# Kernel tuning notes

Hardware: AMD Instinct MI355X
Metric: run time of the kernel (lower is better)

Reference implementation:

```python
import jax, jax.numpy as jnp
import numpy as np

T_STEPS, BATCH, DX, DH = 128, 128, 1024, 1024
N_GATES = 5


def setup_inputs() -> dict:
    key = jax.random.key(0)
    ks = jax.random.split(key, 4)
    scale_x = 1.0 / np.sqrt(DX)
    scale_h = 1.0 / np.sqrt(DH)
    inputs = jax.random.normal(ks[0], (T_STEPS, BATCH, DX), dtype=jnp.float32)
    memories = jax.random.normal(ks[1], (T_STEPS, BATCH, DH), dtype=jnp.float32)
    h0 = jnp.zeros((BATCH, DH), dtype=jnp.float32)
    c0 = jnp.zeros((BATCH, DH), dtype=jnp.float32)
    Wx = jax.random.normal(ks[2], (N_GATES * DH, DX), dtype=jnp.float32) * scale_x
    bx = jnp.zeros((N_GATES * DH,), dtype=jnp.float32)
    Wh = jax.random.normal(ks[3], (N_GATES * DH, DH), dtype=jnp.float32) * scale_h
    # forget-gate bias (second chunk) initialized to 1, as in reset_parameters_
    bh = jnp.zeros((N_GATES * DH,), dtype=jnp.float32).at[DH:2 * DH].set(1.0)
    return {"inputs": inputs, "memories": memories, "h0": h0, "c0": c0,
            "Wx": Wx, "bx": bx, "Wh": Wh, "bh": bh}


def reference(inputs, memories, h0, c0, Wx, bx, Wh, bh):
    # EpLSTMCell.loop: time-major scan of the custom gated cell.
    # Gate order: I, F, G, O, R (tied forget gate: it = 1 - ft).
    def step(carry, inp):
        h, c = carry
        xt, mt = inp
        gx = jnp.dot(xt, Wx.T) + bx      # [B, 5*Dh]
        gh = jnp.dot(h, Wh.T) + bh       # [B, 5*Dh]
        Xi, Xf, Xg, Xo, Xr = jnp.split(gx, N_GATES, axis=-1)
        Hi, Hf, Hg, Ho, Hr = jnp.split(gh, N_GATES, axis=-1)
        ft = jax.nn.sigmoid(Xf + Hf)
        ot = jax.nn.sigmoid(Xo + Ho)
        it = 1.0 - ft                    # tied forget gate
        gt = jnp.tanh(Xg + Hg)
        rt = jax.nn.sigmoid(Xr + Hr)     # episodic memory gate
        ct = ft * c + it * gt + rt * jnp.tanh(mt)
        ht = ot * jnp.tanh(ct)
        return (ht, ct), ht

    (_, _), outs = jax.lax.scan(step, (h0, c0), (inputs, memories))
    return outs  # [T, B, Dh]
```

## Files before the change

kernel.cpp:

```cpp
#include <hip/hip_runtime.h>

#define T_STEPS 128
#define BATCH   128
#define DX      1024
#define DH      1024
#define BDH     (BATCH * DH)
#define BDX     (BATCH * DX)

typedef __attribute__((ext_vector_type(8)))  short short8;
typedef __attribute__((ext_vector_type(16))) float f32x16;

static __device__ __forceinline__ unsigned short f2bf(float f) {
    union { float f; unsigned u; } v; v.f = f;
    unsigned r = v.u + 0x7fffu + ((v.u >> 16) & 1u);
    return (unsigned short)(r >> 16);
}

__global__ __launch_bounds__(256) void prep_x(const float* __restrict__ x,
                                              unsigned short* __restrict__ Xb) {
    const size_t i8 = ((size_t)blockIdx.x * 256 + threadIdx.x) * 8;
    float4 lo = reinterpret_cast<const float4*>(x + i8)[0];
    float4 hi = reinterpret_cast<const float4*>(x + i8)[1];
    union { unsigned short u[8]; short8 v; } pk;
    pk.u[0]=f2bf(lo.x); pk.u[1]=f2bf(lo.y); pk.u[2]=f2bf(lo.z); pk.u[3]=f2bf(lo.w);
    pk.u[4]=f2bf(hi.x); pk.u[5]=f2bf(hi.y); pk.u[6]=f2bf(hi.z); pk.u[7]=f2bf(hi.w);
    *reinterpret_cast<short8*>(Xb + i8) = pk.v;
}

__global__ __launch_bounds__(256) void init_seed(const float* __restrict__ h0,
                                                 unsigned short* __restrict__ hseq,
                                                 unsigned* __restrict__ bar) {
    const int i = blockIdx.x * 256 + threadIdx.x;
    hseq[i] = f2bf(h0[i]);
    if (blockIdx.x == 0 && threadIdx.x < 128) bar[threadIdx.x] = 0;
}

template<bool XBF16>
__global__ __launch_bounds__(256, 1) void eplstm_persistent(
    const void*  __restrict__ xsrc,
    const float* __restrict__ mem,
    const float* __restrict__ Wx,
    const float* __restrict__ Wh,
    const float* __restrict__ bxp,
    const float* __restrict__ bhp,
    const float* __restrict__ c0,
    unsigned short* __restrict__ hseq,
    float* __restrict__ out,
    unsigned* __restrict__ bar)
{
    extern __shared__ char smem[];
    float* pl = reinterpret_cast<float*>(smem + 131072);

    const int bid = blockIdx.x;
    const int js  = bid >> 1;
    const int bhh = bid & 1;
    const int tid = threadIdx.x;

    {
        const int prow = tid >> 3;
        const int g = prow >> 3, jj = prow & 7;
        const int srow = (g + 1) * 1024 + js * 8 + jj;
        const int kc = (tid & 7) * 256;
        const int sw = (prow & 7) << 4;
        for (int it = 0; it < 32; ++it) {
            const int k = kc + it * 8;
            const float* src = (k < DX) ? (Wx + (size_t)srow * DX + k)
                                        : (Wh + (size_t)srow * DH + (k - DX));
            float4 lo = reinterpret_cast<const float4*>(src)[0];
            float4 hi = reinterpret_cast<const float4*>(src)[1];
            union { unsigned short u[8]; short8 v; } pk;
            pk.u[0]=f2bf(lo.x); pk.u[1]=f2bf(lo.y); pk.u[2]=f2bf(lo.z); pk.u[3]=f2bf(lo.w);
            pk.u[4]=f2bf(hi.x); pk.u[5]=f2bf(hi.y); pk.u[6]=f2bf(hi.z); pk.u[7]=f2bf(hi.w);
            *reinterpret_cast<short8*>(smem + prow * 4096 + ((k * 2) ^ sw)) = pk.v;
        }
    }

    const int e0   = tid * 2;
    const int bl   = e0 >> 3;
    const int jj0  = e0 & 7;
    const int brow_g = bhh * 64 + bl;
    const size_t oidx = (size_t)brow_g * DH + js * 8 + jj0;
    float biasv[2][4];
    #pragma unroll
    for (int e2 = 0; e2 < 2; ++e2)
        #pragma unroll
        for (int g = 0; g < 4; ++g) {
            const int srow = (g + 1) * 1024 + js * 8 + jj0 + e2;
            biasv[e2][g] = bxp[srow] + bhp[srow];
        }
    float2 creg = *reinterpret_cast<const float2*>(c0 + oidx);
    const int mh_e = bl >> 5, rr = bl & 31;

    const int wave = tid >> 6;
    const int lane = tid & 63;
    const int mh = wave >> 1, kh = wave & 1;
    const int arow   = bhh * 64 + mh * 32 + (lane & 31);
    const int k8     = (lane >> 5) * 8;
    const int brow   = lane & 31;
    const char* bbase = smem + brow * 4096;
    const int swz    = (brow & 7) << 4;
    const int kbyte0 = kh * 2048 + k8 * 2;

    __syncthreads();

    for (int t = 0; t < T_STEPS; ++t) {
        f32x16 ac0 = {}, ac1 = {}, ac2 = {}, ac3 = {};
        if (XBF16 || kh == 1) {
            const unsigned short* Ab = kh
                ? (hseq + (size_t)t * BDH + (size_t)arow * DH + k8)
                : ((const unsigned short*)xsrc + (size_t)t * BDX + (size_t)arow * DX + k8);
            #pragma unroll 8
            for (int ks = 0; ks < 64; ++ks) {
                short8 a = *reinterpret_cast<const short8*>(Ab + ks * 16);
                short8 b = *reinterpret_cast<const short8*>(bbase + ((kbyte0 + ks * 32) ^ swz));
                if      ((ks & 3) == 0) ac0 = __builtin_amdgcn_mfma_f32_32x32x16_bf16(a, b, ac0, 0, 0, 0);
                else if ((ks & 3) == 1) ac1 = __builtin_amdgcn_mfma_f32_32x32x16_bf16(a, b, ac1, 0, 0, 0);
                else if ((ks & 3) == 2) ac2 = __builtin_amdgcn_mfma_f32_32x32x16_bf16(a, b, ac2, 0, 0, 0);
                else                    ac3 = __builtin_amdgcn_mfma_f32_32x32x16_bf16(a, b, ac3, 0, 0, 0);
            }
        } else {
            const float* Af = (const float*)xsrc + (size_t)t * BDX + (size_t)arow * DX + k8;
            #pragma unroll 4
            for (int ks = 0; ks < 64; ++ks) {
                float4 lo = reinterpret_cast<const float4*>(Af + ks * 16)[0];
                float4 hi = reinterpret_cast<const float4*>(Af + ks * 16)[1];
                union { unsigned short u[8]; short8 v; } pk;
                pk.u[0]=f2bf(lo.x); pk.u[1]=f2bf(lo.y); pk.u[2]=f2bf(lo.z); pk.u[3]=f2bf(lo.w);
                pk.u[4]=f2bf(hi.x); pk.u[5]=f2bf(hi.y); pk.u[6]=f2bf(hi.z); pk.u[7]=f2bf(hi.w);
                short8 a = pk.v;
                short8 b = *reinterpret_cast<const short8*>(bbase + ((kbyte0 + ks * 32) ^ swz));
                if      ((ks & 3) == 0) ac0 = __builtin_amdgcn_mfma_f32_32x32x16_bf16(a, b, ac0, 0, 0, 0);
                else if ((ks & 3) == 1) ac1 = __builtin_amdgcn_mfma_f32_32x32x16_bf16(a, b, ac1, 0, 0, 0);
                else if ((ks & 3) == 2) ac2 = __builtin_amdgcn_mfma_f32_32x32x16_bf16(a, b, ac2, 0, 0, 0);
                else                    ac3 = __builtin_amdgcn_mfma_f32_32x32x16_bf16(a, b, ac3, 0, 0, 0);
            }
        }
        f32x16 r = (ac0 + ac1) + (ac2 + ac3);

        #pragma unroll
        for (int i = 0; i < 16; ++i) {
            const int row = (i & 3) + 8 * (i >> 2) + 4 * (lane >> 5);
            pl[(wave * 32 + row) * 33 + brow] = r[i];
        }
        __syncthreads();

        const float2 mt2 = *reinterpret_cast<const float2*>(
            mem + (size_t)t * BDH + oidx);
        float hv[2];
        #pragma unroll
        for (int e2 = 0; e2 < 2; ++e2) {
            const int jj = jj0 + e2;
            float gs[4];
            #pragma unroll
            for (int g = 0; g < 4; ++g) {
                const int col = g * 8 + jj;
                gs[g] = pl[((mh_e * 2 + 0) * 32 + rr) * 33 + col]
                      + pl[((mh_e * 2 + 1) * 32 + rr) * 33 + col]
                      + biasv[e2][g];
            }
            const float ft = 1.f / (1.f + expf(-gs[0]));
            const float gt = tanhf(gs[1]);
            const float ot = 1.f / (1.f + expf(-gs[2]));
            const float rt = 1.f / (1.f + expf(-gs[3]));
            const float cin = e2 ? creg.y : creg.x;
            const float mv  = e2 ? mt2.y : mt2.x;
            const float cv = ft * cin + (1.f - ft) * gt + rt * tanhf(mv);
            if (e2) creg.y = cv; else creg.x = cv;
            hv[e2] = ot * tanhf(cv);
        }
        *reinterpret_cast<float2*>(out + (size_t)t * BDH + oidx) = make_float2(hv[0], hv[1]);
        const unsigned hp = (unsigned)f2bf(hv[0]) | ((unsigned)f2bf(hv[1]) << 16);
        __hip_atomic_store((unsigned*)(hseq + (size_t)(t + 1) * BDH + oidx), hp,
                           __ATOMIC_RELAXED, __HIP_MEMORY_SCOPE_AGENT);

        __syncthreads();
        if (t < T_STEPS - 1) {
            if (tid == 0) {
                const unsigned want = (unsigned)(t + 1);
                const unsigned arrived = __hip_atomic_fetch_add(
                    &bar[bhh * 32], 1u, __ATOMIC_RELAXED, __HIP_MEMORY_SCOPE_AGENT);
                if (arrived == want * 128u - 1u) {
                    __hip_atomic_store(&bar[64 + bhh * 32], want,
                                       __ATOMIC_RELAXED, __HIP_MEMORY_SCOPE_AGENT);
                } else {
                    while (__hip_atomic_load(&bar[64 + bhh * 32],
                                             __ATOMIC_RELAXED, __HIP_MEMORY_SCOPE_AGENT) < want)
                        __builtin_amdgcn_s_sleep(2);
                }
            }
            __syncthreads();
        }
    }
}

extern "C" void kernel_launch(void* const* d_in, const int* in_sizes, int n_in,
                              void* d_out, int out_size, void* d_ws, size_t ws_size,
                              hipStream_t stream) {
    const float* inputs   = (const float*)d_in[0];
    const float* memories = (const float*)d_in[1];
    const float* h0       = (const float*)d_in[2];
    const float* c0       = (const float*)d_in[3];
    const float* Wx       = (const float*)d_in[4];
    const float* bx       = (const float*)d_in[5];
    const float* Wh       = (const float*)d_in[6];
    const float* bh_      = (const float*)d_in[7];
    float* outp = (float*)d_out;

    char* ws = (char*)d_ws;
    size_t off = 0;
    auto alloc = [&](size_t bytes) {
        char* p = ws + off;
        off = (off + bytes + 255) & ~(size_t)255;
        return p;
    };
    unsigned*       bar  = (unsigned*)alloc(128 * sizeof(unsigned));
    unsigned short* hseq = (unsigned short*)alloc((size_t)(T_STEPS + 1) * BDH * 2);
    const size_t x_need = (size_t)T_STEPS * BDX * 2;
    const bool use_xb = (ws_size >= off + x_need + 256);
    unsigned short* Xb = use_xb ? (unsigned short*)alloc(x_need) : nullptr;

    init_seed<<<512, 256, 0, stream>>>(h0, hseq, bar);
    if (use_xb) prep_x<<<8192, 256, 0, stream>>>(inputs, Xb);

    const unsigned smem_bytes = 131072 + 4 * 32 * 33 * 4;
    const void* xsrc = use_xb ? (const void*)Xb : (const void*)inputs;

    if (use_xb) {
        (void)hipFuncSetAttribute((const void*)eplstm_persistent<true>,
                                  hipFuncAttributeMaxDynamicSharedMemorySize, smem_bytes);
        void* kargs[] = { (void*)&xsrc, (void*)&memories, (void*)&Wx, (void*)&Wh,
                          (void*)&bx, (void*)&bh_, (void*)&c0, (void*)&hseq,
                          (void*)&outp, (void*)&bar };
        hipError_t err = hipLaunchCooperativeKernel(
            (const void*)eplstm_persistent<true>, dim3(256), dim3(256),
            kargs, smem_bytes, stream);
        if (err != hipSuccess) {
            eplstm_persistent<true><<<256, 256, smem_bytes, stream>>>(
                xsrc, memories, Wx, Wh, bx, bh_, c0, hseq, outp, bar);
        }
    } else {
        (void)hipFuncSetAttribute((const void*)eplstm_persistent<false>,
                                  hipFuncAttributeMaxDynamicSharedMemorySize, smem_bytes);
        void* kargs[] = { (void*)&xsrc, (void*)&memories, (void*)&Wx, (void*)&Wh,
                          (void*)&bx, (void*)&bh_, (void*)&c0, (void*)&hseq,
                          (void*)&outp, (void*)&bar };
        hipError_t err = hipLaunchCooperativeKernel(
            (const void*)eplstm_persistent<false>, dim3(256), dim3(256),
            kargs, smem_bytes, stream);
        if (err != hipSuccess) {
            eplstm_persistent<false><<<256, 256, smem_bytes, stream>>>(
                xsrc, memories, Wx, Wh, bx, bh_, c0, hseq, outp, bar);
        }
    }
}
```

Baseline: 1.664 ms.

## Hoist input projection into parallel GEMM prepass and pipeline recurrent kernel

Computes the input-to-gate projection for all timesteps ahead of the recurrence in a separate, fully parallel bf16 MFMA GEMM, storing results in fp16 with the combined biases folded in. The persistent recurrent kernel then only performs the hidden-state GEMM against a 64KB bf16 Wh slice, which removes the per-step x-projection from the serial critical path. It also replaces the grid barrier with per-block flag polling, split by batch half, and uses faster exp-based sigmoid and tanh. The cost is an extra pass over a large Gx buffer and reduced gate precision from fp16 storage.

New measurement: 3.140 ms. +88.7%, slower.

```diff
diff --git a/kernel.cpp b/kernel.cpp
--- a/kernel.cpp
+++ b/kernel.cpp
@@ -6,6 +6,7 @@
 #define DH      1024
 #define BDH     (BATCH * DH)
 #define BDX     (BATCH * DX)
+#define PLW     40
 
 typedef __attribute__((ext_vector_type(8)))  short short8;
 typedef __attribute__((ext_vector_type(16))) float f32x16;
@@ -15,6 +16,17 @@
     unsigned r = v.u + 0x7fffu + ((v.u >> 16) & 1u);
     return (unsigned short)(r >> 16);
 }
+static __device__ __forceinline__ float sigf(float x) {
+    float u = __expf(-fabsf(x));
+    float b = 1.0f / (1.0f + u);
+    return x >= 0.0f ? b : 1.0f - b;
+}
+static __device__ __forceinline__ float tanhfast(float x) {
+    float u = __expf(-2.0f * fabsf(x));
+    float r = (1.0f - u) / (1.0f + u);
+    return x >= 0.0f ? r : -r;
+}
+
 
 __global__ __launch_bounds__(256) void prep_x(const float* __restrict__ x,
                                               unsigned short* __restrict__ Xb) {
@@ -29,23 +41,253 @@
 
 __global__ __launch_bounds__(256) void init_seed(const float* __restrict__ h0,
                                                  unsigned short* __restrict__ hseq,
-                                                 unsigned* __restrict__ bar) {
+                                                 unsigned* __restrict__ gflag) {
     const int i = blockIdx.x * 256 + threadIdx.x;
-    hseq[i] = f2bf(h0[i]);
-    if (blockIdx.x == 0 && threadIdx.x < 128) bar[threadIdx.x] = 0;
+    if (i < BDH) hseq[i] = f2bf(h0[i]);
+    if (blockIdx.x == 0) gflag[threadIdx.x] = 0;
+}
+
+__global__ __launch_bounds__(128) void prep_wxp(const float* __restrict__ Wx,
+                                                const float* __restrict__ bx,
+                                                const float* __restrict__ bh,
+                                                unsigned short* __restrict__ Wxp,
+                                                float* __restrict__ bp) {
+    const int p = blockIdx.x;
+    const int js = p >> 5, g = (p >> 3) & 3, jj = p & 7;
+    const int srow = (g + 1) * 1024 + js * 8 + jj;
+    const int k = threadIdx.x * 8;
+    float4 lo = *(const float4*)(Wx + (size_t)srow * DX + k);
+    float4 hi = *(const float4*)(Wx + (size_t)srow * DX + k + 4);
+    union { unsigned short u[8]; short8 v; } pk;
+    pk.u[0]=f2bf(lo.x); pk.u[1]=f2bf(lo.y); pk.u[2]=f2bf(lo.z); pk.u[3]=f2bf(lo.w);
+    pk.u[4]=f2bf(hi.x); pk.u[5]=f2bf(hi.y); pk.u[6]=f2bf(hi.z); pk.u[7]=f2bf(hi.w);
+    *reinterpret_cast<short8*>(Wxp + (size_t)p * 1024 + k) = pk.v;
+    if (threadIdx.x == 0) bp[p] = bx[srow] + bh[srow];
+}
+
+template<bool XBF16>
+__global__ __launch_bounds__(256, 2) void gx_prepass(
+    const void* __restrict__ xsrc, const unsigned short* __restrict__ Wxp,
+    const float* __restrict__ bp, _Float16* __restrict__ Gx)
+{
+    __shared__ char smem[65536];
+    const int bid = blockIdx.x;
+    const int c = bid & 7;
+    const int i = bid >> 3;
+    const int mt = c * 16 + (i >> 7);
+    const int js = i & 127;
+    const int tid = threadIdx.x;
+
+    {
+        const int row = tid >> 3;
+        const int sw = (row & 7) << 4;
+        const unsigned short* src = Wxp + (size_t)(js * 32 + row) * 1024 + (tid & 7) * 128;
+        char* dst = smem + row * 2048;
+        #pragma unroll
+        for (int it = 0; it < 16; ++it) {
+            short8 v = *(const short8*)(src + it * 8);
+            *(short8*)(dst + ((((tid & 7) * 256) + it * 16) ^ sw)) = v;
+        }
+    }
+    __syncthreads();
+
+    const int wave = tid >> 6, lane = tid & 63;
+    const int arow = mt * 128 + wave * 32 + (lane & 31);
+    const int k8 = (lane >> 5) * 8;
+    const char* wrow = smem + (lane & 31) * 2048;
+    const int sw2 = ((lane & 31) & 7) << 4;
+    f32x16 a0 = {}, a1 = {};
+
+    if (XBF16) {
+        const unsigned short* xp = (const unsigned short*)xsrc + (size_t)arow * 1024 + k8;
+        #pragma unroll 8
+        for (int ks = 0; ks < 64; ++ks) {
+            short8 a = *(const short8*)(xp + ks * 16);
+            short8 b = *(const short8*)(wrow + ((ks * 32 + k8 * 2) ^ sw2));
+            if (ks & 1) a1 = __builtin_amdgcn_mfma_f32_32x32x16_bf16(a, b, a1, 0, 0, 0);
+            else        a0 = __builtin_amdgcn_mfma_f32_32x32x16_bf16(a, b, a0, 0, 0, 0);
+        }
+    } else {
+        const float* Af = (const float*)xsrc + (size_t)arow * 1024 + k8;
+        #pragma unroll 8
+        for (int ks = 0; ks < 64; ++ks) {
+            float4 lo = *(const float4*)(Af + ks * 16);
+            float4 hi = *(const float4*)(Af + ks * 16 + 4);
+            union { unsigned u32[4]; short8 v; } pk;
+            pk.u32[0] = __builtin_amdgcn_perm(__float_as_uint(lo.y), __float_as_uint(lo.x), 0x07060302u);
+            pk.u32[1] = __builtin_amdgcn_perm(__float_as_uint(lo.w), __float_as_uint(lo.z), 0x07060302u);
+            pk.u32[2] = __builtin_amdgcn_perm(__float_as_uint(hi.y), __float_as_uint(hi.x), 0x07060302u);
+            pk.u32[3] = __builtin_amdgcn_perm(__float_as_uint(hi.w), __float_as_uint(hi.z), 0x07060302u);
+            short8 b = *(const short8*)(wrow + ((ks * 32 + k8 * 2) ^ sw2));
+            if (ks & 1) a1 = __builtin_amdgcn_mfma_f32_32x32x16_bf16(pk.v, b, a1, 0, 0, 0);
+            else        a0 = __builtin_amdgcn_mfma_f32_32x32x16_bf16(pk.v, b, a0, 0, 0, 0);
+        }
+    }
+    f32x16 r = a0 + a1;
+    __syncthreads();
+
+    float* pl = (float*)smem;
+    #pragma unroll
+    for (int ii = 0; ii < 16; ++ii) {
+        const int rowc = (ii & 3) + 8 * (ii >> 2) + 4 * (lane >> 5);
+        pl[(wave * 32 + rowc) * 33 + (lane & 31)] = r[ii];
+    }
+    __syncthreads();
+
+    {
+        const int p0 = tid * 4;
+        const int row = p0 >> 3;
+        const int jjb = p0 & 7;
+        __attribute__((aligned(16))) _Float16 vals[16];
+        #pragma unroll
+        for (int q = 0; q < 4; ++q) {
+            const int jj = jjb + q;
+            #pragma unroll
+            for (int g = 0; g < 4; ++g) {
+                float v = pl[row * 33 + g * 8 + jj] + bp[js * 32 + g * 8 + jj];
+                vals[q * 4 + g] = (_Float16)v;
+            }
+        }
+        _Float16* dst = Gx + ((size_t)(mt * 128 + row) * 4096 + js * 32 + jjb * 4);
+        *(uint4*)dst       = *(uint4*)&vals[0];
+        *(uint4*)(dst + 8) = *(uint4*)&vals[8];
+    }
+}
+
+__global__ __launch_bounds__(256, 1) void eplstm_h(
+    const _Float16* __restrict__ Gx,  const float* __restrict__ mem,
+    const float* __restrict__ Wh,     const float* __restrict__ c0,
+    unsigned short* __restrict__ hseq, float* __restrict__ out,
+    unsigned* __restrict__ gflag)
+{
+    extern __shared__ char smem[];
+    float* pl = (float*)(smem + 65536);
+
+    const int bid = blockIdx.x;
+    const int js = bid >> 1, bhh = bid & 1;
+    const int tid = threadIdx.x;
+
+    {
+        const int row = tid >> 3;
+        const int g = row >> 3, jj = row & 7;
+        const int srow = (g + 1) * 1024 + js * 8 + jj;
+        const int sw = (row & 7) << 4;
+        const float* W = Wh + (size_t)srow * 1024;
+        char* dst = smem + row * 2048;
+        #pragma unroll
+        for (int it = 0; it < 16; ++it) {
+            const int k = (tid & 7) * 128 + it * 8;
+            float4 lo = *(const float4*)(W + k);
+            float4 hi = *(const float4*)(W + k + 4);
+            union { unsigned short u[8]; short8 v; } pk;
+            pk.u[0]=f2bf(lo.x); pk.u[1]=f2bf(lo.y); pk.u[2]=f2bf(lo.z); pk.u[3]=f2bf(lo.w);
+            pk.u[4]=f2bf(hi.x); pk.u[5]=f2bf(hi.y); pk.u[6]=f2bf(hi.z); pk.u[7]=f2bf(hi.w);
+            *(short8*)(dst + ((k * 2) ^ sw)) = pk.v;
+        }
+    }
+
+    const int e0 = tid * 2;
+    const int row_e = e0 >> 3;
+    const int jj0 = e0 & 7;
+    const int brow = bhh * 64 + row_e;
+    const size_t obase = (size_t)brow * DH + js * 8 + jj0;
+    const int mh_e = row_e >> 5, r_e = row_e & 31;
+    float2 creg = *(const float2*)(c0 + obase);
+
+    const int wave = tid >> 6, lane = tid & 63;
+    const int mh = wave >> 1, kh = wave & 1;
+    const int arow = bhh * 64 + mh * 32 + (lane & 31);
+    const int k8 = (lane >> 5) * 8;
+    const char* wrow = smem + (lane & 31) * 2048;
+    const int sw2 = ((lane & 31) & 7) << 4;
+    const int kbyte0 = (kh * 512 + k8) * 2;
+    const int p = lane & 31;
+    const int word = (p & 7) * 4 + (p >> 3);
+    float* plw = pl + wave * 32 * PLW;
+    unsigned long long* fb = (unsigned long long*)(gflag + bhh * 128);
+
+    __syncthreads();
+
+    for (int t = 0; t < T_STEPS; ++t) {
+        uint4 gxv = *(const uint4*)(Gx + ((size_t)(t * BATCH + brow) * 4096 + js * 32 + jj0 * 4));
+        float2 mv = *(const float2*)(mem + (size_t)t * BDH + obase);
+
+        if (t > 0) {
+            for (;;) {
+                unsigned long long fv = __hip_atomic_load(&fb[lane], __ATOMIC_RELAXED,
+                                                          __HIP_MEMORY_SCOPE_AGENT);
+                if (__all(((unsigned)fv >= (unsigned)t) &&
+                          ((unsigned)(fv >> 32) >= (unsigned)t))) break;
+                __builtin_amdgcn_s_sleep(2);
+            }
+        }
+
+        const unsigned short* hp = hseq + (size_t)t * BDH + (size_t)arow * DH + kh * 512 + k8;
+        f32x16 a0 = {}, a1 = {};
+        #pragma unroll 16
+        for (int ks = 0; ks < 32; ++ks) {
+            short8 a = *(const short8*)(hp + ks * 16);
+            short8 b = *(const short8*)(wrow + ((kbyte0 + ks * 32) ^ sw2));
+            if (ks & 1) a1 = __builtin_amdgcn_mfma_f32_32x32x16_bf16(a, b, a1, 0, 0, 0);
+            else        a0 = __builtin_amdgcn_mfma_f32_32x32x16_bf16(a, b, a0, 0, 0, 0);
+        }
+        f32x16 r = a0 + a1;
+        #pragma unroll
+        for (int ii = 0; ii < 16; ++ii) {
+            const int rowc = (ii & 3) + 8 * (ii >> 2) + 4 * (lane >> 5);
+            plw[rowc * PLW + word] = r[ii];
+        }
+        __syncthreads();
+
+        float4 p0A = *(const float4*)(pl + (((mh_e << 1) | 0) * 32 + r_e) * PLW + (jj0 + 0) * 4);
+        float4 p0B = *(const float4*)(pl + (((mh_e << 1) | 1) * 32 + r_e) * PLW + (jj0 + 0) * 4);
+        float4 p1A = *(const float4*)(pl + (((mh_e << 1) | 0) * 32 + r_e) * PLW + (jj0 + 1) * 4);
+        float4 p1B = *(const float4*)(pl + (((mh_e << 1) | 1) * 32 + r_e) * PLW + (jj0 + 1) * 4);
+        union { uint4 u; _Float16 h[8]; } G; G.u = gxv;
+
+        float hv[2];
+        {
+            const float gF = (float)G.h[0] + p0A.x + p0B.x;
+            const float gG = (float)G.h[1] + p0A.y + p0B.y;
+            const float gO = (float)G.h[2] + p0A.z + p0B.z;
+            const float gR = (float)G.h[3] + p0A.w + p0B.w;
+            const float ft = sigf(gF), ot = sigf(gO), rt = sigf(gR);
+            const float gt = tanhfast(gG);
+            const float cv = ft * creg.x + (1.f - ft) * gt + rt * tanhfast(mv.x);
+            creg.x = cv;
+            hv[0] = ot * tanhfast(cv);
+        }
+        {
+            const float gF = (float)G.h[4] + p1A.x + p1B.x;
+            const float gG = (float)G.h[5] + p1A.y + p1B.y;
+            const float gO = (float)G.h[6] + p1A.z + p1B.z;
+            const float gR = (float)G.h[7] + p1A.w + p1B.w;
+            const float ft = sigf(gF), ot = sigf(gO), rt = sigf(gR);
+            const float gt = tanhfast(gG);
+            const float cv = ft * creg.y + (1.f - ft) * gt + rt * tanhfast(mv.y);
+            creg.y = cv;
+            hv[1] = ot * tanhfast(cv);
+        }
+        *(float2*)(out + (size_t)t * BDH + obase) = make_float2(hv[0], hv[1]);
+        const unsigned hp2 = (unsigned)f2bf(hv[0]) | ((unsigned)f2bf(hv[1]) << 16);
+        __hip_atomic_store((unsigned*)(hseq + (size_t)(t + 1) * BDH + obase), hp2,
+                           __ATOMIC_RELAXED, __HIP_MEMORY_SCOPE_AGENT);
+
+        __syncthreads();
+        if (tid == 0 && t < T_STEPS - 1) {
+            __hip_atomic_store(&gflag[bhh * 128 + js], (unsigned)(t + 1),
+                               __ATOMIC_RELEASE, __HIP_MEMORY_SCOPE_AGENT);
+        }
+    }
 }
 
 template<bool XBF16>
 __global__ __launch_bounds__(256, 1) void eplstm_persistent(
-    const void*  __restrict__ xsrc,
-    const float* __restrict__ mem,
-    const float* __restrict__ Wx,
-    const float* __restrict__ Wh,
-    const float* __restrict__ bxp,
-    const float* __restrict__ bhp,
+    const void*  __restrict__ xsrc, const float* __restrict__ mem,
+    const float* __restrict__ Wx,   const float* __restrict__ Wh,
+    const float* __restrict__ bxp,  const float* __restrict__ bhp,
     const float* __restrict__ c0,
-    unsigned short* __restrict__ hseq,
-    float* __restrict__ out,
+    unsigned short* __restrict__ hseq, float* __restrict__ out,
     unsigned* __restrict__ bar)
 {
     extern __shared__ char smem[];
@@ -144,8 +386,7 @@
         }
         __syncthreads();
 
-        const float2 mt2 = *reinterpret_cast<const float2*>(
-            mem + (size_t)t * BDH + oidx);
+        const float2 mt2 = *reinterpret_cast<const float2*>(mem + (size_t)t * BDH + oidx);
         float hv[2];
         #pragma unroll
         for (int e2 = 0; e2 < 2; ++e2) {
@@ -213,43 +454,78 @@
         off = (off + bytes + 255) & ~(size_t)255;
         return p;
     };
-    unsigned*       bar  = (unsigned*)alloc(128 * sizeof(unsigned));
-    unsigned short* hseq = (unsigned short*)alloc((size_t)(T_STEPS + 1) * BDH * 2);
-    const size_t x_need = (size_t)T_STEPS * BDX * 2;
-    const bool use_xb = (ws_size >= off + x_need + 256);
-    unsigned short* Xb = use_xb ? (unsigned short*)alloc(x_need) : nullptr;
-
-    init_seed<<<512, 256, 0, stream>>>(h0, hseq, bar);
-    if (use_xb) prep_x<<<8192, 256, 0, stream>>>(inputs, Xb);
-
-    const unsigned smem_bytes = 131072 + 4 * 32 * 33 * 4;
-    const void* xsrc = use_xb ? (const void*)Xb : (const void*)inputs;
-
-    if (use_xb) {
-        (void)hipFuncSetAttribute((const void*)eplstm_persistent<true>,
+    unsigned*       gflag = (unsigned*)alloc(256 * sizeof(unsigned));
+    unsigned short* hseq  = (unsigned short*)alloc((size_t)(T_STEPS + 1) * BDH * 2);
+
+    const size_t wxp_b  = (size_t)4096 * 1024 * 2;
+    const size_t bp_b   = 4096 * 4;
+    const size_t gx_b   = (size_t)16384 * 4096 * 2;
+    const size_t xb_b   = (size_t)T_STEPS * BDX * 2;
+    const size_t need_base = off + wxp_b + 256 + bp_b + 256 + gx_b + 256;
+    const size_t need_xb   = need_base + xb_b + 256;
+
+    if (ws_size >= need_base) {
+        unsigned short* Wxp = (unsigned short*)alloc(wxp_b);
+        float*          bp  = (float*)alloc(bp_b);
+        _Float16*       Gx  = (_Float16*)alloc(gx_b);
+        const bool use_xb = (ws_size >= need_xb);
+        unsigned short* Xb = use_xb ? (unsigned short*)alloc(xb_b) : nullptr;
+
+        init_seed<<<512, 256, 0, stream>>>(h0, hseq, gflag);
+        prep_wxp<<<4096, 128, 0, stream>>>(Wx, bx, bh_, Wxp, bp);
+        if (use_xb) {
+            prep_x<<<8192, 256, 0, stream>>>(inputs, Xb);
+            gx_prepass<true><<<16384, 256, 0, stream>>>((const void*)Xb, Wxp, bp, Gx);
+        } else {
+            gx_prepass<false><<<16384, 256, 0, stream>>>((const void*)inputs, Wxp, bp, Gx);
+        }
+
+        const unsigned smem_bytes = 65536 + 4 * 32 * PLW * 4;
+        (void)hipFuncSetAttribute((const void*)eplstm_h,
                                   hipFuncAttributeMaxDynamicSharedMemorySize, smem_bytes);
-        void* kargs[] = { (void*)&xsrc, (void*)&memories, (void*)&Wx, (void*)&Wh,
-                          (void*)&bx, (void*)&bh_, (void*)&c0, (void*)&hseq,
-                          (void*)&outp, (void*)&bar };
-        hipError_t err = hipLaunchCooperativeKernel(
-            (const void*)eplstm_persistent<true>, dim3(256), dim3(256),
-            kargs, smem_bytes, stream);
+        void* kargs[] = { (void*)&Gx, (void*)&memories, (void*)&Wh, (void*)&c0,
+                          (void*)&hseq, (void*)&outp, (void*)&gflag };
+        hipError_t err = hipLaunchCooperativeKernel((const void*)eplstm_h, dim3(256),
+                                                    dim3(256), kargs, smem_bytes, stream);
         if (err != hipSuccess) {
-            eplstm_persistent<true><<<256, 256, smem_bytes, stream>>>(
-                xsrc, memories, Wx, Wh, bx, bh_, c0, hseq, outp, bar);
+            eplstm_h<<<256, 256, smem_bytes, stream>>>(Gx, memories, Wh, c0,
+                                                       hseq, outp, gflag);
         }
     } else {
-        (void)hipFuncSetAttribute((const void*)eplstm_persistent<false>,
-                                  hipFuncAttributeMaxDynamicSharedMemorySize, smem_bytes);
-        void* kargs[] = { (void*)&xsrc, (void*)&memories, (void*)&Wx, (void*)&Wh,
-                          (void*)&bx, (void*)&bh_, (void*)&c0, (void*)&hseq,
-                          (void*)&outp, (void*)&bar };
-        hipError_t err = hipLaunchCooperativeKernel(
-            (const void*)eplstm_persistent<false>, dim3(256), dim3(256),
-            kargs, smem_bytes, stream);
-        if (err != hipSuccess) {
-            eplstm_persistent<false><<<256, 256, smem_bytes, stream>>>(
-                xsrc, memories, Wx, Wh, bx, bh_, c0, hseq, outp, bar);
-        }
-    }
-}
+        const bool use_xb = (ws_size >= off + xb_b + 256);
+        unsigned short* Xb = use_xb ? (unsigned short*)alloc(xb_b) : nullptr;
+
+        init_seed<<<512, 256, 0, stream>>>(h0, hseq, gflag);
+        if (use_xb) prep_x<<<8192, 256, 0, stream>>>(inputs, Xb);
+
+        const unsigned smem_bytes = 131072 + 9216 + 9216 + 64;
+        const void* xsrc = use_xb ? (const void*)Xb : (const void*)inputs;
+        if (use_xb) {
+            (void)hipFuncSetAttribute((const void*)eplstm_persistent<true>,
+                                      hipFuncAttributeMaxDynamicSharedMemorySize, smem_bytes);
+            void* kargs[] = { (void*)&xsrc, (void*)&memories, (void*)&Wx, (void*)&Wh,
+                              (void*)&bx, (void*)&bh_, (void*)&c0, (void*)&hseq,
+                              (void*)&outp, (void*)&gflag };
+            hipError_t err = hipLaunchCooperativeKernel(
+                (const void*)eplstm_persistent<true>, dim3(256), dim3(256),
+                kargs, smem_bytes, stream);
+            if (err != hipSuccess) {
+                eplstm_persistent<true><<<256, 256, smem_bytes, stream>>>(
+                    xsrc, memories, Wx, Wh, bx, bh_, c0, hseq, outp, gflag);
+            }
+        } else {
+            (void)hipFuncSetAttribute((const void*)eplstm_persistent<false>,
+                                      hipFuncAttributeMaxDynamicSharedMemorySize, smem_bytes);
+            void* kargs[] = { (void*)&xsrc, (void*)&memories, (void*)&Wx, (void*)&Wh,
+                              (void*)&bx, (void*)&bh_, (void*)&c0, (void*)&hseq,
+                              (void*)&outp, (void*)&gflag };
+            hipError_t err = hipLaunchCooperativeKernel(
+                (const void*)eplstm_persistent<false>, dim3(256), dim3(256),
+                kargs, smem_bytes, stream);
+            if (err != hipSuccess) {
+                eplstm_persistent<false><<<256, 256, smem_bytes, stream>>>(
+                    xsrc, memories, Wx, Wh, bx, bh_, c0, hseq, outp, gflag);
+            }
+        }
+    }
+}
```
